# Kernel tuning notes

Hardware: AMD Instinct MI355X
Metric: run time of the kernel (lower is better)

## Reference

```python
import jax, jax.numpy as jnp
import numpy as np

NEG_SLOPE = 0.2  # PyG GATConv default LeakyReLU slope


def _gat(h, src, dst, num_nodes, W, a_src, a_dst, bias):
    """PyG-style GATConv (concat=True, eval mode, self-loops already in src/dst)."""
    heads, out = a_src.shape
    hp = (h @ W).reshape(num_nodes, heads, out)          # (N, H, F)
    e_s = (hp * a_src).sum(-1)                            # (N, H)
    e_d = (hp * a_dst).sum(-1)                            # (N, H)
    e = jax.nn.leaky_relu(e_s[src] + e_d[dst], NEG_SLOPE)  # (E, H)
    m = jax.ops.segment_max(e, dst, num_segments=num_nodes)
    w = jnp.exp(e - m[dst])
    z = jax.ops.segment_sum(w, dst, num_segments=num_nodes)
    alpha = w / (z[dst] + 1e-16)                          # softmax over in-edges per dst
    agg = jax.ops.segment_sum(hp[src] * alpha[:, :, None], dst, num_segments=num_nodes)
    return agg.reshape(num_nodes, heads * out) + bias


def setup_inputs() -> dict:
    key = jax.random.key(0)
    ks = jax.random.split(key, 20)
    N, T, Fin, H, heads, E = 30000, 4, 256, 64, 4, 240000
    D = H * heads  # 256
    s = 0.05
    p = lambda k, shape: (jax.random.normal(k, shape, jnp.float32) * s)
    return {
        "x": jax.random.normal(ks[0], (N, T, Fin), jnp.float32),
        "edge_index": jax.random.randint(ks[1], (2, E), 0, N, jnp.int32),
        "Wp": p(ks[2], (Fin, H)), "bp": p(ks[3], (H,)),
        "W0": p(ks[4], (H, D)), "a_src0": p(ks[5], (heads, H)), "a_dst0": p(ks[6], (heads, H)), "b0": p(ks[7], (D,)),
        "W1": p(ks[8], (D, D)), "a_src1": p(ks[9], (heads, H)), "a_dst1": p(ks[10], (heads, H)), "b1": p(ks[11], (D,)),
        "Wq": p(ks[12], (D, D)), "bq": p(ks[13], (D,)),
        "Wk": p(ks[14], (D, D)), "bk": p(ks[15], (D,)),
        "Wv": p(ks[16], (D, D)), "bv": p(ks[17], (D,)),
    }


def reference(x, edge_index, Wp, bp, W0, a_src0, a_dst0, b0, W1, a_src1, a_dst1, b1,
              Wq, bq, Wk, bk, Wv, bv):
    N, T, Fin = x.shape
    D = Wq.shape[0]
    loops = jnp.arange(N, dtype=edge_index.dtype)
    src = jnp.concatenate([edge_index[0], loops])  # add self-loops (PyG default)
    dst = jnp.concatenate([edge_index[1], loops])
    xT = jnp.transpose(x, (1, 0, 2))  # (T, N, Fin)

    def step(_, xt):
        h = xt @ Wp + bp
        h = jax.nn.elu(_gat(h, src, dst, N, W0, a_src0, a_dst0, b0))
        h = jax.nn.elu(_gat(h, src, dst, N, W1, a_src1, a_dst1, b1))
        return None, h

    _, embs = jax.lax.scan(step, None, xT)  # (T, N, D)

    # temporal attention
    Q = embs @ Wq + bq
    K = embs @ Wk + bk
    V = embs @ Wv + bv
    Q_time = Q.mean(axis=1)  # (T, D)
    K_time = K.mean(axis=1)  # (T, D)
    scores = (Q_time @ K_time.T) / jnp.sqrt(jnp.asarray(D, jnp.float32))
    attn = jax.nn.softmax(scores, axis=1)            # (T, T)
    Vr = V.reshape(T, -1)                            # (T, N*D)
    attended = attn @ Vr                             # (T, N*D)
    return attended[-1].reshape(N, D)
```

## Files before the change

### kernel.cpp

```cpp
#include <hip/hip_runtime.h>
#include <math.h>

#define NEG_SLOPE 0.2f

typedef __attribute__((ext_vector_type(8))) short short8;
typedef __attribute__((ext_vector_type(4))) float f32x4;

__device__ inline unsigned short f2bf(float f){
  union { float f; unsigned u; } v; v.f = f;
  unsigned r = v.u + 0x7fffu + ((v.u >> 16) & 1u);
  return (unsigned short)(r >> 16);
}
__device__ inline float bf2f(unsigned u){
  union { unsigned u; float f; } v; v.u = u << 16; return v.f;
}

__global__ __launch_bounds__(256) void k_deg_count(const int* __restrict__ dst, int E, int* __restrict__ deg){
  int i = blockIdx.x*256 + threadIdx.x;
  if (i < E) atomicAdd(&deg[dst[i]], 1);
}
__global__ __launch_bounds__(256) void k_scan_blk(const int* __restrict__ deg, int* __restrict__ rowptr,
                                                  int* __restrict__ bsum, int N){
  __shared__ int ws[4];
  int tid = threadIdx.x;
  int i = blockIdx.x*256 + tid;
  int v = (i < N) ? deg[i]+1 : 0;
  int lane = tid & 63, w = tid >> 6;
  int s = v;
  #pragma unroll
  for (int off=1; off<64; off<<=1){
    int u = __shfl_up(s, off);
    if (lane >= off) s += u;
  }
  if (lane == 63) ws[w] = s;
  __syncthreads();
  int woff = 0;
  #pragma unroll
  for (int k=0;k<4;k++) if (k < w) woff += ws[k];
  int incl = s + woff;
  if (i < N) rowptr[i] = incl - v;
  if (tid == 255) bsum[blockIdx.x] = incl;
}
__global__ __launch_bounds__(256) void k_scan_top(int* __restrict__ bsum, int nb, int* __restrict__ rowptrN){
  __shared__ int buf[256];
  int tid = threadIdx.x;
  int v = (tid < nb) ? bsum[tid] : 0;
  buf[tid] = v;
  __syncthreads();
  for (int off=1; off<256; off<<=1){
    int add = (tid >= off) ? buf[tid-off] : 0;
    __syncthreads();
    buf[tid] += add;
    __syncthreads();
  }
  if (tid < nb) bsum[tid] = buf[tid] - v;
  if (tid == 0) rowptrN[0] = buf[255];
}
__global__ __launch_bounds__(256) void k_scan_fix(int* __restrict__ rowptr, const int* __restrict__ bsum,
                                                  int* __restrict__ pos, int* __restrict__ colidx, int N){
  int i = blockIdx.x*256 + threadIdx.x;
  if (i < N){
    int r = rowptr[i] + bsum[blockIdx.x];
    rowptr[i] = r;
    colidx[r] = i;
    pos[i] = r + 1;
  }
}
__global__ __launch_bounds__(256) void k_fill_edges(const int* __restrict__ src, const int* __restrict__ dst,
                                                    int E, int* __restrict__ pos, int* __restrict__ colidx){
  int i = blockIdx.x*256 + threadIdx.x;
  if (i < E){
    int d = dst[i];
    colidx[atomicAdd(&pos[d],1)] = src[i];
  }
}

__global__ __launch_bounds__(256) void k_prep(const float* __restrict__ Wp, const float* __restrict__ W0,
                                              const float* __restrict__ W1, const float* __restrict__ Wv,
                                              const float* __restrict__ as0, const float* __restrict__ ad0,
                                              unsigned short* __restrict__ WpT, unsigned short* __restrict__ W0T4,
                                              unsigned short* __restrict__ W1T, unsigned short* __restrict__ WvT,
                                              float* __restrict__ ahs, float* __restrict__ ahd){
  int idx = blockIdx.x*256 + threadIdx.x;
  if (idx < 16384){
    int k = idx >> 6, p = idx & 63;
    WpT[p*256 + k] = f2bf(Wp[idx]);
  } else if (idx < 32768){
    int i = idx - 16384;
    int h = i >> 12, r = i & 4095, p = r >> 6, k = r & 63;
    W0T4[i] = f2bf(W0[k*256 + h*64 + p]);
  } else if (idx < 98304){
    int i = idx - 32768; int k = i >> 8, p = i & 255;
    W1T[p*256 + k] = f2bf(W1[i]);
  } else if (idx < 163840){
    int i = idx - 98304; int k = i >> 8, p = i & 255;
    WvT[p*256 + k] = f2bf(Wv[i]);
  } else if (idx < 164096){
    int i = idx - 163840;
    int h = i >> 6, d = i & 63;
    float ss = 0.f, sd = 0.f;
    for (int j=0;j<64;j++){
      float w = W0[d*256 + h*64 + j];
      ss += w * as0[h*64 + j];
      sd += w * ad0[h*64 + j];
    }
    ahs[i] = ss; ahd[i] = sd;
  }
}

__global__ __launch_bounds__(256) void k_h0(const float* __restrict__ A,
                                            const unsigned short* __restrict__ Bt,
                                            const float* __restrict__ bias,
                                            unsigned short* __restrict__ C, int M, int Nn){
  int wid = blockIdx.x*4 + (threadIdx.x >> 6);
  int m0 = wid * 64;
  if (m0 >= M) return;
  int lane = threadIdx.x & 63;
  int lr = lane & 15, g = lane >> 4, lk = g*8;
  const float* Arow[4];
  #pragma unroll
  for (int m=0;m<4;m++){
    int row = m0 + m*16 + lr;
    if (row > M-1) row = M-1;
    Arow[m] = A + (size_t)row*256 + lk;
  }
  const unsigned short* Bb = Bt + (size_t)lr*256 + lk;
  f32x4 acc[4][4];
  #pragma unroll
  for (int m=0;m<4;m++)
    #pragma unroll
    for (int n=0;n<4;n++)
      #pragma unroll
      for (int j=0;j<4;j++) acc[m][n][j] = 0.f;

  #pragma unroll 2
  for (int ks=0; ks<8; ks++){
    int k0 = ks*32;
    short8 bfr[4];
    #pragma unroll
    for (int n=0;n<4;n++)
      bfr[n] = *(const short8*)(Bb + (size_t)n*16*256 + k0);
    short8 afr[4];
    #pragma unroll
    for (int m=0;m<4;m++){
      float4 u = *(const float4*)(Arow[m] + k0);
      float4 w = *(const float4*)(Arow[m] + k0 + 4);
      afr[m][0]=(short)f2bf(u.x); afr[m][1]=(short)f2bf(u.y);
      afr[m][2]=(short)f2bf(u.z); afr[m][3]=(short)f2bf(u.w);
      afr[m][4]=(short)f2bf(w.x); afr[m][5]=(short)f2bf(w.y);
      afr[m][6]=(short)f2bf(w.z); afr[m][7]=(short)f2bf(w.w);
    }
    #pragma unroll
    for (int m=0;m<4;m++)
      #pragma unroll
      for (int n=0;n<4;n++)
        acc[m][n] = __builtin_amdgcn_mfma_f32_16x16x32_bf16(afr[m], bfr[n], acc[m][n], 0,0,0);
  }
  #pragma unroll
  for (int n=0;n<4;n++){
    int col = n*16 + lr;
    float bcol = bias[col];
    #pragma unroll
    for (int m=0;m<4;m++){
      #pragma unroll
      for (int j=0;j<4;j++){
        int row = m0 + m*16 + g*4 + j;
        if (row < M){
          int t = row & 3, nn = row >> 2;
          C[(size_t)t*Nn*64 + (size_t)nn*64 + col] = f2bf(acc[m][n][j] + bcol);
        }
      }
    }
  }
}

__global__ __launch_bounds__(256) void k_gat0(const unsigned short* __restrict__ A,
                                              const unsigned short* __restrict__ W0T4,
                                              const float* __restrict__ b0,
                                              unsigned short* __restrict__ C, int M){
  int h = blockIdx.y;
  int wid = blockIdx.x*4 + (threadIdx.x >> 6);
  int m0 = wid * 64;
  if (m0 >= M) return;
  int lane = threadIdx.x & 63;
  int lr = lane & 15, g = lane >> 4, lk = g*8;
  const unsigned short* Wh = W0T4 + (size_t)h*64*64;
  f32x4 acc[4][4];
  #pragma unroll
  for (int m=0;m<4;m++)
    #pragma unroll
    for (int n=0;n<4;n++)
      #pragma unroll
      for (int j=0;j<4;j++) acc[m][n][j] = 0.f;

  #pragma unroll
  for (int ks=0; ks<2; ks++){
    short8 bfr[4], afr[4];
    #pragma unroll
    for (int n=0;n<4;n++)
      bfr[n] = *(const short8*)(Wh + (size_t)(n*16+lr)*64 + ks*32 + lk);
    #pragma unroll
    for (int m=0;m<4;m++){
      int row = m0 + m*16 + lr;
      if (row > M-1) row = M-1;
      afr[m] = *(const short8*)(A + (size_t)row*256 + h*64 + ks*32 + lk);
    }
    #pragma unroll
    for (int m=0;m<4;m++)
      #pragma unroll
      for (int n=0;n<4;n++)
        acc[m][n] = __builtin_amdgcn_mfma_f32_16x16x32_bf16(afr[m], bfr[n], acc[m][n], 0,0,0);
  }
  #pragma unroll
  for (int n=0;n<4;n++){
    int col = h*64 + n*16 + lr;
    float bcol = b0[col];
    #pragma unroll
    for (int m=0;m<4;m++){
      #pragma unroll
      for (int j=0;j<4;j++){
        int row = m0 + m*16 + g*4 + j;
        if (row < M){
          float v = acc[m][n][j] + bcol;
          v = (v > 0.f) ? v : (__expf(v) - 1.f);
          C[(size_t)row*256 + col] = f2bf(v);
        }
      }
    }
  }
}

template<int K, bool BIAS, bool CF32>
__global__ __launch_bounds__(512) void k_gemm_p256(const unsigned short* __restrict__ A,
                                                   const unsigned short* __restrict__ Bt,
                                                   const float* __restrict__ bias,
                                                   void* __restrict__ Cv, int M){
  constexpr int BK = 64, PAD = 8;
  __shared__ unsigned short Als[128][BK+PAD];
  __shared__ unsigned short Bls[256][BK+PAD];
  int tid = threadIdx.x;
  int m0  = blockIdx.x * 128;
  int wave = tid >> 6, lane = tid & 63;
  int wr = wave & 3, wc = wave >> 2;
  int lr = lane & 15, lk = (lane >> 4) * 8;
  f32x4 acc[2][8];
  #pragma unroll
  for (int m=0;m<2;m++)
    #pragma unroll
    for (int n=0;n<8;n++)
      #pragma unroll
      for (int j=0;j<4;j++) acc[m][n][j] = 0.f;

  for (int k0 = 0; k0 < K; k0 += BK){
    #pragma unroll
    for (int i=0;i<2;i++){
      int idx = tid + i*512;
      int r = idx >> 3, ch = (idx & 7)*8;
      int row = m0 + r;
      uint4 v = make_uint4(0,0,0,0);
      if (row < M) v = *(const uint4*)(A + (size_t)row*K + k0 + ch);
      *(uint4*)(&Als[r][ch]) = v;
    }
    #pragma unroll
    for (int i=0;i<4;i++){
      int idx = tid + i*512;
      int r = idx >> 3, ch = (idx & 7)*8;
      *(uint4*)(&Bls[r][ch]) = *(const uint4*)(Bt + (size_t)r*K + k0 + ch);
    }
    __syncthreads();
    #pragma unroll
    for (int ks=0; ks<2; ks++){
      short8 afr[2], bfr[8];
      #pragma unroll
      for (int m=0;m<2;m++)
        afr[m] = *(const short8*)(&Als[wr*32 + m*16 + lr][ks*32 + lk]);
      #pragma unroll
      for (int n=0;n<8;n++)
        bfr[n] = *(const short8*)(&Bls[wc*128 + n*16 + lr][ks*32 + lk]);
      #pragma unroll
      for (int m=0;m<2;m++)
        #pragma unroll
        for (int n=0;n<8;n++)
          acc[m][n] = __builtin_amdgcn_mfma_f32_16x16x32_bf16(afr[m], bfr[n], acc[m][n], 0,0,0);
    }
    __syncthreads();
  }
  #pragma unroll
  for (int m=0;m<2;m++){
    #pragma unroll
    for (int n=0;n<8;n++){
      int col = wc*128 + n*16 + lr;
      float bcol = BIAS ? bias[col] : 0.f;
      #pragma unroll
      for (int j=0;j<4;j++){
        int row = m0 + wr*32 + m*16 + (lane>>4)*4 + j;
        if (row < M){
          float v = acc[m][n][j] + bcol;
          if (CF32) ((float*)Cv)[(size_t)row*256 + col] = v;
          else      ((unsigned short*)Cv)[(size_t)row*256 + col] = f2bf(v);
        }
      }
    }
  }
}

__global__ __launch_bounds__(512) void k_gemm_fin(const unsigned short* __restrict__ embs,
                                                  const float* __restrict__ awp,
                                                  const unsigned short* __restrict__ Bt,
                                                  const float* __restrict__ bias,
                                                  float* __restrict__ C, int M){
  constexpr int K = 256, BK = 64, PAD = 8;
  __shared__ unsigned short Als[128][BK+PAD];
  __shared__ unsigned short Bls[256][BK+PAD];
  int tid = threadIdx.x;
  int m0  = blockIdx.x * 128;
  int wave = tid >> 6, lane = tid & 63;
  int wr = wave & 3, wc = wave >> 2;
  int lr = lane & 15, lk = (lane >> 4) * 8;
  float a0=awp[0], a1=awp[1], a2=awp[2], a3=awp[3];
  size_t sl = (size_t)M*256;
  f32x4 acc[2][8];
  #pragma unroll
  for (int m=0;m<2;m++)
    #pragma unroll
    for (int n=0;n<8;n++)
      #pragma unroll
      for (int j=0;j<4;j++) acc[m][n][j] = 0.f;

  for (int k0 = 0; k0 < K; k0 += BK){
    #pragma unroll
    for (int i=0;i<2;i++){
      int idx = tid + i*512;
      int r = idx >> 3, ch = (idx & 7)*8;
      int row = m0 + r;
      uint4 w = make_uint4(0,0,0,0);
      if (row < M){
        size_t o = (size_t)row*256 + k0 + ch;
        uint4 u0 = *(const uint4*)(embs + o);
        uint4 u1 = *(const uint4*)(embs + o + sl);
        uint4 u2 = *(const uint4*)(embs + o + 2*sl);
        uint4 u3 = *(const uint4*)(embs + o + 3*sl);
        const unsigned* p0=&u0.x; const unsigned* p1=&u1.x;
        const unsigned* p2=&u2.x; const unsigned* p3=&u3.x;
        unsigned* pw=&w.x;
        #pragma unroll
        for (int q=0;q<4;q++){
          float lo = a0*bf2f(p0[q]&0xffffu) + a1*bf2f(p1[q]&0xffffu) + a2*bf2f(p2[q]&0xffffu) + a3*bf2f(p3[q]&0xffffu);
          float hi = a0*bf2f(p0[q]>>16)     + a1*bf2f(p1[q]>>16)     + a2*bf2f(p2[q]>>16)     + a3*bf2f(p3[q]>>16);
          pw[q] = (unsigned)f2bf(lo) | ((unsigned)f2bf(hi) << 16);
        }
      }
      *(uint4*)(&Als[r][ch]) = w;
    }
    #pragma unroll
    for (int i=0;i<4;i++){
      int idx = tid + i*512;
      int r = idx >> 3, ch = (idx & 7)*8;
      *(uint4*)(&Bls[r][ch]) = *(const uint4*)(Bt + (size_t)r*K + k0 + ch);
    }
    __syncthreads();
    #pragma unroll
    for (int ks=0; ks<2; ks++){
      short8 afr[2], bfr[8];
      #pragma unroll
      for (int m=0;m<2;m++)
        afr[m] = *(const short8*)(&Als[wr*32 + m*16 + lr][ks*32 + lk]);
      #pragma unroll
      for (int n=0;n<8;n++)
        bfr[n] = *(const short8*)(&Bls[wc*128 + n*16 + lr][ks*32 + lk]);
      #pragma unroll
      for (int m=0;m<2;m++)
        #pragma unroll
        for (int n=0;n<8;n++)
          acc[m][n] = __builtin_amdgcn_mfma_f32_16x16x32_bf16(afr[m], bfr[n], acc[m][n], 0,0,0);
    }
    __syncthreads();
  }
  #pragma unroll
  for (int m=0;m<2;m++){
    #pragma unroll
    for (int n=0;n<8;n++){
      int col = wc*128 + n*16 + lr;
      float bcol = bias[col];
      #pragma unroll
      for (int j=0;j<4;j++){
        int row = m0 + wr*32 + m*16 + (lane>>4)*4 + j;
        if (row < M)
          C[(size_t)row*256 + col] = acc[m][n][j] + bcol;
      }
    }
  }
}

__global__ __launch_bounds__(256) void k_esd0(const unsigned short* __restrict__ h0,
                                              const float* __restrict__ ahs, const float* __restrict__ ahd,
                                              float* __restrict__ e_s, float* __restrict__ e_d, int M){
  int n = blockIdx.x*4 + (threadIdx.x >> 6);
  if (n >= M) return;
  int lane = threadIdx.x & 63;
  int h = lane >> 4, l4 = (lane & 15)*4;
  uint2 v = *(const uint2*)(h0 + (size_t)n*64 + l4);
  float v0 = bf2f(v.x & 0xffffu), v1 = bf2f(v.x >> 16);
  float v2 = bf2f(v.y & 0xffffu), v3 = bf2f(v.y >> 16);
  float4 as = *(const float4*)(ahs + h*64 + l4);
  float4 ad = *(const float4*)(ahd + h*64 + l4);
  float ps = v0*as.x + v1*as.y + v2*as.z + v3*as.w;
  float pd = v0*ad.x + v1*ad.y + v2*ad.z + v3*ad.w;
  #pragma unroll
  for (int off=1; off<16; off<<=1){ ps += __shfl_xor(ps,off); pd += __shfl_xor(pd,off); }
  if ((lane & 15) == 0){
    e_s[n*4+h] = ps; e_d[n*4+h] = pd;
  }
}

__global__ __launch_bounds__(256) void k_agg0(const unsigned short* __restrict__ h0all,
                                              const float* __restrict__ e_s, const float* __restrict__ e_d,
                                              const int* __restrict__ rowptr, const int* __restrict__ colidx,
                                              unsigned short* __restrict__ agg, int N){
  int n = blockIdx.x*4 + (threadIdx.x >> 6);
  if (n >= N) return;
  int t = blockIdx.y;
  int g = t*N + n;
  int lane = threadIdx.x & 63;
  int h = lane >> 4, l4 = (lane & 15)*4;
  int s0 = rowptr[n], s1 = rowptr[n+1];
  float ed = e_d[(size_t)g*4 + h];
  float z = 0.f;
  float a0=0.f, a1=0.f, a2=0.f, a3=0.f;
  const unsigned short* h0t = h0all + (size_t)t*N*64;
  const float* est = e_s + (size_t)t*N*4;
  int i = s0;
  for (; i+4 <= s1; i += 4){
    int sA = colidx[i], sB = colidx[i+1], sC = colidx[i+2], sD = colidx[i+3];
    uint2 vA = *(const uint2*)(h0t + (size_t)sA*64 + l4);
    uint2 vB = *(const uint2*)(h0t + (size_t)sB*64 + l4);
    uint2 vC = *(const uint2*)(h0t + (size_t)sC*64 + l4);
    uint2 vD = *(const uint2*)(h0t + (size_t)sD*64 + l4);
    float eA = est[sA*4+h] + ed, eB = est[sB*4+h] + ed, eC = est[sC*4+h] + ed, eD = est[sD*4+h] + ed;
    eA = (eA>0.f)?eA:NEG_SLOPE*eA; eB = (eB>0.f)?eB:NEG_SLOPE*eB;
    eC = (eC>0.f)?eC:NEG_SLOPE*eC; eD = (eD>0.f)?eD:NEG_SLOPE*eD;
    float wA = __expf(eA), wB = __expf(eB), wC = __expf(eC), wD = __expf(eD);
    z += (wA + wB) + (wC + wD);
    a0 += wA*bf2f(vA.x&0xffffu) + wB*bf2f(vB.x&0xffffu) + wC*bf2f(vC.x&0xffffu) + wD*bf2f(vD.x&0xffffu);
    a1 += wA*bf2f(vA.x>>16)     + wB*bf2f(vB.x>>16)     + wC*bf2f(vC.x>>16)     + wD*bf2f(vD.x>>16);
    a2 += wA*bf2f(vA.y&0xffffu) + wB*bf2f(vB.y&0xffffu) + wC*bf2f(vC.y&0xffffu) + wD*bf2f(vD.y&0xffffu);
    a3 += wA*bf2f(vA.y>>16)     + wB*bf2f(vB.y>>16)     + wC*bf2f(vC.y>>16)     + wD*bf2f(vD.y>>16);
  }
  for (; i < s1; ++i){
    int s = colidx[i];
    float e = est[s*4 + h] + ed;
    e = (e > 0.f) ? e : NEG_SLOPE*e;
    float w = __expf(e);
    z += w;
    uint2 v = *(const uint2*)(h0t + (size_t)s*64 + l4);
    a0 += w * bf2f(v.x & 0xffffu);
    a1 += w * bf2f(v.x >> 16);
    a2 += w * bf2f(v.y & 0xffffu);
    a3 += w * bf2f(v.y >> 16);
  }
  float inv = 1.f / (z + 1e-16f);
  unsigned lo = (unsigned)f2bf(a0*inv) | ((unsigned)f2bf(a1*inv) << 16);
  unsigned hi = (unsigned)f2bf(a2*inv) | ((unsigned)f2bf(a3*inv) << 16);
  *(uint2*)(agg + (size_t)g*256 + h*64 + l4) = make_uint2(lo, hi);
}

__global__ __launch_bounds__(256) void k_esd(const unsigned short* __restrict__ hp,
                                             const float* __restrict__ a_s, const float* __restrict__ a_d,
                                             float* __restrict__ e_s, float* __restrict__ e_d, int M){
  int n = blockIdx.x*4 + (threadIdx.x >> 6);
  if (n >= M) return;
  int lane = threadIdx.x & 63;
  uint2 v = *(const uint2*)(hp + (size_t)n*256 + lane*4);
  float v0 = bf2f(v.x & 0xffffu), v1 = bf2f(v.x >> 16);
  float v2 = bf2f(v.y & 0xffffu), v3 = bf2f(v.y >> 16);
  float4 as = *(const float4*)(a_s + lane*4);
  float4 ad = *(const float4*)(a_d + lane*4);
  float ps = v0*as.x + v1*as.y + v2*as.z + v3*as.w;
  float pd = v0*ad.x + v1*ad.y + v2*ad.z + v3*ad.w;
  #pragma unroll
  for (int off=1; off<16; off<<=1){ ps += __shfl_xor(ps,off); pd += __shfl_xor(pd,off); }
  if ((lane & 15) == 0){
    int h = lane >> 4;
    e_s[n*4+h] = ps; e_d[n*4+h] = pd;
  }
}

__global__ __launch_bounds__(256) void k_agg(const unsigned short* __restrict__ hpall,
                                             const float* __restrict__ e_s, const float* __restrict__ e_d,
                                             const int* __restrict__ rowptr, const int* __restrict__ colidx,
                                             const float* __restrict__ bias, unsigned short* __restrict__ outb,
                                             int N){
  int n = blockIdx.x*4 + (threadIdx.x >> 6);
  if (n >= N) return;
  int t = blockIdx.y;
  int g = t*N + n;
  int lane = threadIdx.x & 63;
  int h = lane >> 4;
  int s0 = rowptr[n], s1 = rowptr[n+1];
  float ed = e_d[(size_t)g*4 + h];
  float z = 0.f;
  float a0=0.f, a1=0.f, a2=0.f, a3=0.f;
  const unsigned short* hpt = hpall + (size_t)t*N*256;
  const float* est = e_s + (size_t)t*N*4;
  int i = s0;
  for (; i+4 <= s1; i += 4){
    int sA = colidx[i], sB = colidx[i+1], sC = colidx[i+2], sD = colidx[i+3];
    uint2 vA = *(const uint2*)(hpt + (size_t)sA*256 + lane*4);
    uint2 vB = *(const uint2*)(hpt + (size_t)sB*256 + lane*4);
    uint2 vC = *(const uint2*)(hpt + (size_t)sC*256 + lane*4);
    uint2 vD = *(const uint2*)(hpt + (size_t)sD*256 + lane*4);
    float eA = est[sA*4+h] + ed, eB = est[sB*4+h] + ed, eC = est[sC*4+h] + ed, eD = est[sD*4+h] + ed;
    eA = (eA>0.f)?eA:NEG_SLOPE*eA; eB = (eB>0.f)?eB:NEG_SLOPE*eB;
    eC = (eC>0.f)?eC:NEG_SLOPE*eC; eD = (eD>0.f)?eD:NEG_SLOPE*eD;
    float wA = __expf(eA), wB = __expf(eB), wC = __expf(eC), wD = __expf(eD);
    z += (wA + wB) + (wC + wD);
    a0 += wA*bf2f(vA.x&0xffffu) + wB*bf2f(vB.x&0xffffu) + wC*bf2f(vC.x&0xffffu) + wD*bf2f(vD.x&0xffffu);
    a1 += wA*bf2f(vA.x>>16)     + wB*bf2f(vB.x>>16)     + wC*bf2f(vC.x>>16)     + wD*bf2f(vD.x>>16);
    a2 += wA*bf2f(vA.y&0xffffu) + wB*bf2f(vB.y&0xffffu) + wC*bf2f(vC.y&0xffffu) + wD*bf2f(vD.y&0xffffu);
    a3 += wA*bf2f(vA.y>>16)     + wB*bf2f(vB.y>>16)     + wC*bf2f(vC.y>>16)     + wD*bf2f(vD.y>>16);
  }
  for (; i < s1; ++i){
    int s = colidx[i];
    float e = est[s*4 + h] + ed;
    e = (e > 0.f) ? e : NEG_SLOPE*e;
    float w = __expf(e);
    z += w;
    uint2 v = *(const uint2*)(hpt + (size_t)s*256 + lane*4);
    a0 += w * bf2f(v.x & 0xffffu);
    a1 += w * bf2f(v.x >> 16);
    a2 += w * bf2f(v.y & 0xffffu);
    a3 += w * bf2f(v.y >> 16);
  }
  float inv = 1.f / (z + 1e-16f);
  float4 b = *(const float4*)(bias + lane*4);
  float o0 = a0*inv + b.x, o1 = a1*inv + b.y, o2 = a2*inv + b.z, o3 = a3*inv + b.w;
  o0 = (o0 > 0.f) ? o0 : (__expf(o0) - 1.f);
  o1 = (o1 > 0.f) ? o1 : (__expf(o1) - 1.f);
  o2 = (o2 > 0.f) ? o2 : (__expf(o2) - 1.f);
  o3 = (o3 > 0.f) ? o3 : (__expf(o3) - 1.f);
  unsigned lo = (unsigned)f2bf(o0) | ((unsigned)f2bf(o1) << 16);
  unsigned hi = (unsigned)f2bf(o2) | ((unsigned)f2bf(o3) << 16);
  *(uint2*)(outb + (size_t)g*256 + lane*4) = make_uint2(lo, hi);
}

__global__ __launch_bounds__(256) void k_colsum(const unsigned short* __restrict__ emb, float* __restrict__ sums, int N){
  __shared__ float red[8][256];
  int tid = threadIdx.x;
  int t = blockIdx.x >> 6, chunk = blockIdx.x & 63;
  int rows_per = (N + 63) / 64;
  int r0 = chunk * rows_per;
  int r1 = min(N, r0 + rows_per);
  const unsigned short* base = emb + (size_t)t*N*256;
  int c0 = (tid & 31)*8, rg = tid >> 5;
  float s[8] = {0,0,0,0,0,0,0,0};
  for (int r = r0 + rg; r < r1; r += 8){
    uint4 v = *(const uint4*)(base + (size_t)r*256 + c0);
    s[0] += bf2f(v.x & 0xffffu); s[1] += bf2f(v.x >> 16);
    s[2] += bf2f(v.y & 0xffffu); s[3] += bf2f(v.y >> 16);
    s[4] += bf2f(v.z & 0xffffu); s[5] += bf2f(v.z >> 16);
    s[6] += bf2f(v.w & 0xffffu); s[7] += bf2f(v.w >> 16);
  }
  #pragma unroll
  for (int j=0;j<8;j++) red[rg][c0+j] = s[j];
  __syncthreads();
  float tot = 0.f;
  #pragma unroll
  for (int g=0;g<8;g++) tot += red[g][tid];
  atomicAdd(&sums[t*256 + tid], tot);
}

__global__ __launch_bounds__(256) void k_attn(const float* __restrict__ sum_emb,
                                              const float* __restrict__ Wq, const float* __restrict__ bq,
                                              const float* __restrict__ Wk, const float* __restrict__ bk,
                                              float* __restrict__ aw, int N){
  __shared__ float mean_s[4][256];
  __shared__ float red[256];
  __shared__ float scores_s[4];
  int j = threadIdx.x;
  float invN = 1.0f/(float)N;
  #pragma unroll
  for (int t=0;t<4;t++) mean_s[t][j] = sum_emb[t*256+j]*invN;
  __syncthreads();
  float q3 = bq[j];
  float kt0=bk[j], kt1=bk[j], kt2=bk[j], kt3=bk[j];
  for (int m=0;m<256;m++){
    float wq = Wq[m*256+j];
    float wk = Wk[m*256+j];
    float m0 = mean_s[0][m], m1 = mean_s[1][m], m2 = mean_s[2][m], m3 = mean_s[3][m];
    q3  += m3*wq;
    kt0 += m0*wk; kt1 += m1*wk; kt2 += m2*wk; kt3 += m3*wk;
  }
  float kts0=kt0, kts1=kt1, kts2=kt2, kts3=kt3;
  #pragma unroll
  for (int t=0;t<4;t++){
    float ktv = (t==0)?kts0:((t==1)?kts1:((t==2)?kts2:kts3));
    red[j] = q3*ktv;
    __syncthreads();
    for (int off=128; off>0; off>>=1){
      if (j < off) red[j] += red[j+off];
      __syncthreads();
    }
    if (j==0) scores_s[t] = red[0]*(1.0f/16.0f);
    __syncthreads();
  }
  if (j==0){
    float mx = fmaxf(fmaxf(scores_s[0],scores_s[1]),fmaxf(scores_s[2],scores_s[3]));
    float w0 = __expf(scores_s[0]-mx), w1 = __expf(scores_s[1]-mx),
          w2 = __expf(scores_s[2]-mx), w3 = __expf(scores_s[3]-mx);
    float s = w0+w1+w2+w3;
    aw[0]=w0/s; aw[1]=w1/s; aw[2]=w2/s; aw[3]=w3/s;
  }
}

extern "C" void kernel_launch(void* const* d_in, const int* in_sizes, int n_in,
                              void* d_out, int out_size, void* d_ws, size_t ws_size,
                              hipStream_t stream){
  (void)n_in; (void)out_size; (void)ws_size;
  const float* x   = (const float*)d_in[0];
  const int*   ei  = (const int*)d_in[1];
  const float* Wp  = (const float*)d_in[2];
  const float* bp  = (const float*)d_in[3];
  const float* W0  = (const float*)d_in[4];
  const float* as0 = (const float*)d_in[5];
  const float* ad0 = (const float*)d_in[6];
  const float* b0  = (const float*)d_in[7];
  const float* W1  = (const float*)d_in[8];
  const float* as1 = (const float*)d_in[9];
  const float* ad1 = (const float*)d_in[10];
  const float* b1  = (const float*)d_in[11];
  const float* Wq  = (const float*)d_in[12];
  const float* bq  = (const float*)d_in[13];
  const float* Wk  = (const float*)d_in[14];
  const float* bk  = (const float*)d_in[15];
  const float* Wv  = (const float*)d_in[16];
  const float* bv  = (const float*)d_in[17];
  float* out = (float*)d_out;

  const int T = 4, FIN = 256;
  const int N = in_sizes[0] / (T*FIN);
  const int E = in_sizes[1] / 2;
  const int TN = T*N;
  const int* src = ei;
  const int* dst = ei + E;

  char* ws = (char*)d_ws;
  size_t cur = 0;
  auto alloc = [&](size_t bytes)->void*{
    void* p = ws + cur;
    cur += (bytes + 255) & ~(size_t)255;
    return p;
  };
  unsigned short* h0all = (unsigned short*)alloc((size_t)TN*64*2);
  unsigned short* bufA  = (unsigned short*)alloc((size_t)TN*256*2);
  unsigned short* bufB  = (unsigned short*)alloc((size_t)TN*256*2);
  unsigned short* embs  = (unsigned short*)alloc((size_t)TN*256*2);
  float* e_s    = (float*)alloc((size_t)TN*4*4);
  float* e_d    = (float*)alloc((size_t)TN*4*4);
  float* sume   = (float*)alloc(4*256*4);
  float* aw     = (float*)alloc(256);
  float* ah0s   = (float*)alloc(256*4);
  float* ah0d   = (float*)alloc(256*4);
  int*   rowptr = (int*)alloc((size_t)(N+1)*4);
  int*   deg    = (int*)alloc((size_t)N*4);
  int*   pos    = (int*)alloc((size_t)N*4);
  int*   bsum   = (int*)alloc((size_t)256*4);
  int*   colidx = (int*)alloc((size_t)(E+N)*4);
  unsigned short* WpT  = (unsigned short*)alloc((size_t)64*256*2);
  unsigned short* W0T4 = (unsigned short*)alloc((size_t)4*64*64*2);
  unsigned short* W1T  = (unsigned short*)alloc((size_t)256*256*2);
  unsigned short* WvT  = (unsigned short*)alloc((size_t)256*256*2);

  int nb256 = (N+255)/256;
  int nbE   = (E+255)/256;
  int gm4   = (TN+127)/128;
  int gmN   = (N+127)/128;
  int gagg  = (TN+3)/4;

  hipMemsetAsync(deg, 0, (size_t)N*4, stream);
  k_deg_count<<<nbE,256,0,stream>>>(dst, E, deg);
  k_scan_blk<<<nb256,256,0,stream>>>(deg, rowptr, bsum, N);
  k_scan_top<<<1,256,0,stream>>>(bsum, nb256, rowptr + N);
  k_scan_fix<<<nb256,256,0,stream>>>(rowptr, bsum, pos, colidx, N);
  k_fill_edges<<<nbE,256,0,stream>>>(src, dst, E, pos, colidx);
  hipMemsetAsync(sume, 0, 4*256*4, stream);

  k_prep<<<641,256,0,stream>>>(Wp, W0, W1, Wv, as0, ad0, WpT, W0T4, W1T, WvT, ah0s, ah0d);

  k_h0<<<(TN/64+3)/4 + 1,256,0,stream>>>(x, WpT, bp, h0all, TN, N);

  k_esd0<<<gagg,256,0,stream>>>(h0all, ah0s, ah0d, e_s, e_d, TN);
  k_agg0<<<dim3((N+3)/4, T),256,0,stream>>>(h0all, e_s, e_d, rowptr, colidx, bufA, N);
  k_gat0<<<dim3((TN+255)/256, 4),256,0,stream>>>(bufA, W0T4, b0, bufB, TN);
  k_gemm_p256<256,false,false><<<gm4,512,0,stream>>>(bufB, W1T, nullptr, bufA, TN);
  k_esd<<<gagg,256,0,stream>>>(bufA, as1, ad1, e_s, e_d, TN);
  k_agg<<<dim3((N+3)/4, T),256,0,stream>>>(bufA, e_s, e_d, rowptr, colidx, b1, embs, N);
  k_colsum<<<256,256,0,stream>>>(embs, sume, N);

  k_attn<<<1,256,0,stream>>>(sume, Wq, bq, Wk, bk, aw, N);
  k_gemm_fin<<<gmN,512,0,stream>>>(embs, aw, WvT, bv, out, N);
}
```

Measured before the change: 457.4 us.

## Fuse GAT0 projection with layer-1 GEMM and vectorize edge aggregation loops

Merges the per-head layer-0 transform (with bias and ELU) and the layer-1 256x256 projection into one kernel. The intermediate activation tile stays in shared memory, so the bf16 round trip through global memory and one launch go away. The two aggregation kernels now split each wave into two halves that each take alternate edges with 16-byte loads, then combine the halves with a cross-half shuffle. In exchange, the fused kernel uses a smaller 64-row tile and reloads W1 per block, and half the lanes sit idle in the aggregation epilogue.

```diff
diff --git a/kernel.cpp b/kernel.cpp
--- a/kernel.cpp
+++ b/kernel.cpp
@@ -174,132 +174,85 @@
   }
 }
 
-__global__ __launch_bounds__(256) void k_gat0(const unsigned short* __restrict__ A,
-                                              const unsigned short* __restrict__ W0T4,
-                                              const float* __restrict__ b0,
-                                              unsigned short* __restrict__ C, int M){
-  int h = blockIdx.y;
-  int wid = blockIdx.x*4 + (threadIdx.x >> 6);
-  int m0 = wid * 64;
-  if (m0 >= M) return;
-  int lane = threadIdx.x & 63;
-  int lr = lane & 15, g = lane >> 4, lk = g*8;
-  const unsigned short* Wh = W0T4 + (size_t)h*64*64;
-  f32x4 acc[4][4];
-  #pragma unroll
-  for (int m=0;m<4;m++)
-    #pragma unroll
-    for (int n=0;n<4;n++)
-      #pragma unroll
-      for (int j=0;j<4;j++) acc[m][n][j] = 0.f;
-
-  #pragma unroll
-  for (int ks=0; ks<2; ks++){
-    short8 bfr[4], afr[4];
-    #pragma unroll
-    for (int n=0;n<4;n++)
-      bfr[n] = *(const short8*)(Wh + (size_t)(n*16+lr)*64 + ks*32 + lk);
-    #pragma unroll
-    for (int m=0;m<4;m++){
-      int row = m0 + m*16 + lr;
-      if (row > M-1) row = M-1;
-      afr[m] = *(const short8*)(A + (size_t)row*256 + h*64 + ks*32 + lk);
-    }
-    #pragma unroll
-    for (int m=0;m<4;m++)
-      #pragma unroll
-      for (int n=0;n<4;n++)
-        acc[m][n] = __builtin_amdgcn_mfma_f32_16x16x32_bf16(afr[m], bfr[n], acc[m][n], 0,0,0);
-  }
-  #pragma unroll
-  for (int n=0;n<4;n++){
-    int col = h*64 + n*16 + lr;
+__global__ __launch_bounds__(256) void k_gat01(const unsigned short* __restrict__ A,
+                                               const unsigned short* __restrict__ W0T4,
+                                               const float* __restrict__ b0,
+                                               const unsigned short* __restrict__ W1T,
+                                               unsigned short* __restrict__ hp, int M){
+  __shared__ unsigned short H1[64][264];
+  __shared__ unsigned short Bls[256][72];
+  int tid = threadIdx.x;
+  int m0 = blockIdx.x * 64;
+  int wave = tid >> 6, lane = tid & 63;
+  int lr = lane & 15, g4 = lane >> 4, lk = g4*8;
+  int rbase = m0 + wave*16;
+
+  f32x4 acc1[16];
+  #pragma unroll
+  for (int q=0;q<16;q++)
+    #pragma unroll
+    for (int j=0;j<4;j++) acc1[q][j] = 0.f;
+  int arow = rbase + lr; if (arow > M-1) arow = M-1;
+  #pragma unroll
+  for (int h=0;h<4;h++){
+    short8 afr[2];
+    #pragma unroll
+    for (int ks=0;ks<2;ks++)
+      afr[ks] = *(const short8*)(A + (size_t)arow*256 + h*64 + ks*32 + lk);
+    #pragma unroll
+    for (int nn=0;nn<4;nn++){
+      #pragma unroll
+      for (int ks=0;ks<2;ks++){
+        short8 bfr = *(const short8*)(W0T4 + ((size_t)h*64 + nn*16 + lr)*64 + ks*32 + lk);
+        acc1[h*4+nn] = __builtin_amdgcn_mfma_f32_16x16x32_bf16(afr[ks], bfr, acc1[h*4+nn], 0,0,0);
+      }
+    }
+  }
+  #pragma unroll
+  for (int q=0;q<16;q++){
+    int col = q*16 + lr;
     float bcol = b0[col];
     #pragma unroll
-    for (int m=0;m<4;m++){
-      #pragma unroll
-      for (int j=0;j<4;j++){
-        int row = m0 + m*16 + g*4 + j;
-        if (row < M){
-          float v = acc[m][n][j] + bcol;
-          v = (v > 0.f) ? v : (__expf(v) - 1.f);
-          C[(size_t)row*256 + col] = f2bf(v);
-        }
+    for (int j=0;j<4;j++){
+      float v = acc1[q][j] + bcol;
+      v = (v > 0.f) ? v : (__expf(v) - 1.f);
+      H1[wave*16 + g4*4 + j][col] = f2bf(v);
+    }
+  }
+  __syncthreads();
+
+  f32x4 acc2[16];
+  #pragma unroll
+  for (int q=0;q<16;q++)
+    #pragma unroll
+    for (int j=0;j<4;j++) acc2[q][j] = 0.f;
+  for (int k0=0;k0<256;k0+=64){
+    #pragma unroll
+    for (int it=0; it<8; it++){
+      int idx = tid + it*256;
+      int p = idx >> 3, ch = (idx & 7)*8;
+      *(uint4*)(&Bls[p][ch]) = *(const uint4*)(W1T + (size_t)p*256 + k0 + ch);
+    }
+    __syncthreads();
+    #pragma unroll
+    for (int ks=0;ks<2;ks++){
+      short8 afr = *(const short8*)(&H1[wave*16 + lr][k0 + ks*32 + lk]);
+      #pragma unroll
+      for (int q=0;q<16;q++){
+        short8 bfr = *(const short8*)(&Bls[q*16 + lr][ks*32 + lk]);
+        acc2[q] = __builtin_amdgcn_mfma_f32_16x16x32_bf16(afr, bfr, acc2[q], 0,0,0);
       }
     }
-  }
-}
-
-template<int K, bool BIAS, bool CF32>
-__global__ __launch_bounds__(512) void k_gemm_p256(const unsigned short* __restrict__ A,
-                                                   const unsigned short* __restrict__ Bt,
-                                                   const float* __restrict__ bias,
-                                                   void* __restrict__ Cv, int M){
-  constexpr int BK = 64, PAD = 8;
-  __shared__ unsigned short Als[128][BK+PAD];
-  __shared__ unsigned short Bls[256][BK+PAD];
-  int tid = threadIdx.x;
-  int m0  = blockIdx.x * 128;
-  int wave = tid >> 6, lane = tid & 63;
-  int wr = wave & 3, wc = wave >> 2;
-  int lr = lane & 15, lk = (lane >> 4) * 8;
-  f32x4 acc[2][8];
-  #pragma unroll
-  for (int m=0;m<2;m++)
-    #pragma unroll
-    for (int n=0;n<8;n++)
-      #pragma unroll
-      for (int j=0;j<4;j++) acc[m][n][j] = 0.f;
-
-  for (int k0 = 0; k0 < K; k0 += BK){
-    #pragma unroll
-    for (int i=0;i<2;i++){
-      int idx = tid + i*512;
-      int r = idx >> 3, ch = (idx & 7)*8;
-      int row = m0 + r;
-      uint4 v = make_uint4(0,0,0,0);
-      if (row < M) v = *(const uint4*)(A + (size_t)row*K + k0 + ch);
-      *(uint4*)(&Als[r][ch]) = v;
-    }
-    #pragma unroll
-    for (int i=0;i<4;i++){
-      int idx = tid + i*512;
-      int r = idx >> 3, ch = (idx & 7)*8;
-      *(uint4*)(&Bls[r][ch]) = *(const uint4*)(Bt + (size_t)r*K + k0 + ch);
-    }
-    __syncthreads();
-    #pragma unroll
-    for (int ks=0; ks<2; ks++){
-      short8 afr[2], bfr[8];
-      #pragma unroll
-      for (int m=0;m<2;m++)
-        afr[m] = *(const short8*)(&Als[wr*32 + m*16 + lr][ks*32 + lk]);
-      #pragma unroll
-      for (int n=0;n<8;n++)
-        bfr[n] = *(const short8*)(&Bls[wc*128 + n*16 + lr][ks*32 + lk]);
-      #pragma unroll
-      for (int m=0;m<2;m++)
-        #pragma unroll
-        for (int n=0;n<8;n++)
-          acc[m][n] = __builtin_amdgcn_mfma_f32_16x16x32_bf16(afr[m], bfr[n], acc[m][n], 0,0,0);
-    }
-    __syncthreads();
-  }
-  #pragma unroll
-  for (int m=0;m<2;m++){
-    #pragma unroll
-    for (int n=0;n<8;n++){
-      int col = wc*128 + n*16 + lr;
-      float bcol = BIAS ? bias[col] : 0.f;
-      #pragma unroll
-      for (int j=0;j<4;j++){
-        int row = m0 + wr*32 + m*16 + (lane>>4)*4 + j;
-        if (row < M){
-          float v = acc[m][n][j] + bcol;
-          if (CF32) ((float*)Cv)[(size_t)row*256 + col] = v;
-          else      ((unsigned short*)Cv)[(size_t)row*256 + col] = f2bf(v);
-        }
-      }
+    __syncthreads();
+  }
+  #pragma unroll
+  for (int q=0;q<16;q++){
+    int col = q*16 + lr;
+    #pragma unroll
+    for (int j=0;j<4;j++){
+      int row = m0 + wave*16 + g4*4 + j;
+      if (row < M)
+        hp[(size_t)row*256 + col] = f2bf(acc2[q][j]);
     }
   }
 }
@@ -422,46 +375,51 @@
   int t = blockIdx.y;
   int g = t*N + n;
   int lane = threadIdx.x & 63;
-  int h = lane >> 4, l4 = (lane & 15)*4;
+  int half = lane >> 5, l = lane & 31;
+  int h = l >> 3, di = (l & 7)*8;
   int s0 = rowptr[n], s1 = rowptr[n+1];
   float ed = e_d[(size_t)g*4 + h];
-  float z = 0.f;
-  float a0=0.f, a1=0.f, a2=0.f, a3=0.f;
   const unsigned short* h0t = h0all + (size_t)t*N*64;
   const float* est = e_s + (size_t)t*N*4;
+  float z = 0.f;
+  float a[8] = {0,0,0,0,0,0,0,0};
   int i = s0;
-  for (; i+4 <= s1; i += 4){
-    int sA = colidx[i], sB = colidx[i+1], sC = colidx[i+2], sD = colidx[i+3];
-    uint2 vA = *(const uint2*)(h0t + (size_t)sA*64 + l4);
-    uint2 vB = *(const uint2*)(h0t + (size_t)sB*64 + l4);
-    uint2 vC = *(const uint2*)(h0t + (size_t)sC*64 + l4);
-    uint2 vD = *(const uint2*)(h0t + (size_t)sD*64 + l4);
-    float eA = est[sA*4+h] + ed, eB = est[sB*4+h] + ed, eC = est[sC*4+h] + ed, eD = est[sD*4+h] + ed;
-    eA = (eA>0.f)?eA:NEG_SLOPE*eA; eB = (eB>0.f)?eB:NEG_SLOPE*eB;
-    eC = (eC>0.f)?eC:NEG_SLOPE*eC; eD = (eD>0.f)?eD:NEG_SLOPE*eD;
-    float wA = __expf(eA), wB = __expf(eB), wC = __expf(eC), wD = __expf(eD);
-    z += (wA + wB) + (wC + wD);
-    a0 += wA*bf2f(vA.x&0xffffu) + wB*bf2f(vB.x&0xffffu) + wC*bf2f(vC.x&0xffffu) + wD*bf2f(vD.x&0xffffu);
-    a1 += wA*bf2f(vA.x>>16)     + wB*bf2f(vB.x>>16)     + wC*bf2f(vC.x>>16)     + wD*bf2f(vD.x>>16);
-    a2 += wA*bf2f(vA.y&0xffffu) + wB*bf2f(vB.y&0xffffu) + wC*bf2f(vC.y&0xffffu) + wD*bf2f(vD.y&0xffffu);
-    a3 += wA*bf2f(vA.y>>16)     + wB*bf2f(vB.y>>16)     + wC*bf2f(vC.y>>16)     + wD*bf2f(vD.y>>16);
-  }
-  for (; i < s1; ++i){
-    int s = colidx[i];
+  for (; i+2 <= s1; i += 2){
+    int s = colidx[i + half];
+    uint4 v = *(const uint4*)(h0t + (size_t)s*64 + di);
     float e = est[s*4 + h] + ed;
-    e = (e > 0.f) ? e : NEG_SLOPE*e;
+    e = fmaxf(e, NEG_SLOPE*e);
     float w = __expf(e);
     z += w;
-    uint2 v = *(const uint2*)(h0t + (size_t)s*64 + l4);
-    a0 += w * bf2f(v.x & 0xffffu);
-    a1 += w * bf2f(v.x >> 16);
-    a2 += w * bf2f(v.y & 0xffffu);
-    a3 += w * bf2f(v.y >> 16);
-  }
-  float inv = 1.f / (z + 1e-16f);
-  unsigned lo = (unsigned)f2bf(a0*inv) | ((unsigned)f2bf(a1*inv) << 16);
-  unsigned hi = (unsigned)f2bf(a2*inv) | ((unsigned)f2bf(a3*inv) << 16);
-  *(uint2*)(agg + (size_t)g*256 + h*64 + l4) = make_uint2(lo, hi);
+    a[0] += w*bf2f(v.x&0xffffu); a[1] += w*bf2f(v.x>>16);
+    a[2] += w*bf2f(v.y&0xffffu); a[3] += w*bf2f(v.y>>16);
+    a[4] += w*bf2f(v.z&0xffffu); a[5] += w*bf2f(v.z>>16);
+    a[6] += w*bf2f(v.w&0xffffu); a[7] += w*bf2f(v.w>>16);
+  }
+  if (i < s1 && half == 0){
+    int s = colidx[i];
+    uint4 v = *(const uint4*)(h0t + (size_t)s*64 + di);
+    float e = est[s*4 + h] + ed;
+    e = fmaxf(e, NEG_SLOPE*e);
+    float w = __expf(e);
+    z += w;
+    a[0] += w*bf2f(v.x&0xffffu); a[1] += w*bf2f(v.x>>16);
+    a[2] += w*bf2f(v.y&0xffffu); a[3] += w*bf2f(v.y>>16);
+    a[4] += w*bf2f(v.z&0xffffu); a[5] += w*bf2f(v.z>>16);
+    a[6] += w*bf2f(v.w&0xffffu); a[7] += w*bf2f(v.w>>16);
+  }
+  z += __shfl_xor(z, 32);
+  #pragma unroll
+  for (int q=0;q<8;q++) a[q] += __shfl_xor(a[q], 32);
+  if (half == 0){
+    float inv = 1.f / (z + 1e-16f);
+    uint4 r;
+    r.x = (unsigned)f2bf(a[0]*inv) | ((unsigned)f2bf(a[1]*inv) << 16);
+    r.y = (unsigned)f2bf(a[2]*inv) | ((unsigned)f2bf(a[3]*inv) << 16);
+    r.z = (unsigned)f2bf(a[4]*inv) | ((unsigned)f2bf(a[5]*inv) << 16);
+    r.w = (unsigned)f2bf(a[6]*inv) | ((unsigned)f2bf(a[7]*inv) << 16);
+    *(uint4*)(agg + (size_t)g*256 + l*8) = r;
+  }
 }
 
 __global__ __launch_bounds__(256) void k_esd(const unsigned short* __restrict__ hp,
@@ -495,52 +453,58 @@
   int t = blockIdx.y;
   int g = t*N + n;
   int lane = threadIdx.x & 63;
-  int h = lane >> 4;
+  int half = lane >> 5, l = lane & 31;
+  int h = l >> 3, d0 = l*8;
   int s0 = rowptr[n], s1 = rowptr[n+1];
   float ed = e_d[(size_t)g*4 + h];
-  float z = 0.f;
-  float a0=0.f, a1=0.f, a2=0.f, a3=0.f;
   const unsigned short* hpt = hpall + (size_t)t*N*256;
   const float* est = e_s + (size_t)t*N*4;
+  float z = 0.f;
+  float a[8] = {0,0,0,0,0,0,0,0};
   int i = s0;
-  for (; i+4 <= s1; i += 4){
-    int sA = colidx[i], sB = colidx[i+1], sC = colidx[i+2], sD = colidx[i+3];
-    uint2 vA = *(const uint2*)(hpt + (size_t)sA*256 + lane*4);
-    uint2 vB = *(const uint2*)(hpt + (size_t)sB*256 + lane*4);
-    uint2 vC = *(const uint2*)(hpt + (size_t)sC*256 + lane*4);
-    uint2 vD = *(const uint2*)(hpt + (size_t)sD*256 + lane*4);
-    float eA = est[sA*4+h] + ed, eB = est[sB*4+h] + ed, eC = est[sC*4+h] + ed, eD = est[sD*4+h] + ed;
-    eA = (eA>0.f)?eA:NEG_SLOPE*eA; eB = (eB>0.f)?eB:NEG_SLOPE*eB;
-    eC = (eC>0.f)?eC:NEG_SLOPE*eC; eD = (eD>0.f)?eD:NEG_SLOPE*eD;
-    float wA = __expf(eA), wB = __expf(eB), wC = __expf(eC), wD = __expf(eD);
-    z += (wA + wB) + (wC + wD);
-    a0 += wA*bf2f(vA.x&0xffffu) + wB*bf2f(vB.x&0xffffu) + wC*bf2f(vC.x&0xffffu) + wD*bf2f(vD.x&0xffffu);
-    a1 += wA*bf2f(vA.x>>16)     + wB*bf2f(vB.x>>16)     + wC*bf2f(vC.x>>16)     + wD*bf2f(vD.x>>16);
-    a2 += wA*bf2f(vA.y&0xffffu) + wB*bf2f(vB.y&0xffffu) + wC*bf2f(vC.y&0xffffu) + wD*bf2f(vD.y&0xffffu);
-    a3 += wA*bf2f(vA.y>>16)     + wB*bf2f(vB.y>>16)     + wC*bf2f(vC.y>>16)     + wD*bf2f(vD.y>>16);
-  }
-  for (; i < s1; ++i){
-    int s = colidx[i];
+  for (; i+2 <= s1; i += 2){
+    int s = colidx[i + half];
+    uint4 v = *(const uint4*)(hpt + (size_t)s*256 + d0);
     float e = est[s*4 + h] + ed;
-    e = (e > 0.f) ? e : NEG_SLOPE*e;
+    e = fmaxf(e, NEG_SLOPE*e);
     float w = __expf(e);
     z += w;
-    uint2 v = *(const uint2*)(hpt + (size_t)s*256 + lane*4);
-    a0 += w * bf2f(v.x & 0xffffu);
-    a1 += w * bf2f(v.x >> 16);
-    a2 += w * bf2f(v.y & 0xffffu);
-    a3 += w * bf2f(v.y >> 16);
-  }
-  float inv = 1.f / (z + 1e-16f);
-  float4 b = *(const float4*)(bias + lane*4);
-  float o0 = a0*inv + b.x, o1 = a1*inv + b.y, o2 = a2*inv + b.z, o3 = a3*inv + b.w;
-  o0 = (o0 > 0.f) ? o0 : (__expf(o0) - 1.f);
-  o1 = (o1 > 0.f) ? o1 : (__expf(o1) - 1.f);
-  o2 = (o2 > 0.f) ? o2 : (__expf(o2) - 1.f);
-  o3 = (o3 > 0.f) ? o3 : (__expf(o3) - 1.f);
-  unsigned lo = (unsigned)f2bf(o0) | ((unsigned)f2bf(o1) << 16);
-  unsigned hi = (unsigned)f2bf(o2) | ((unsigned)f2bf(o3) << 16);
-  *(uint2*)(outb + (size_t)g*256 + lane*4) = make_uint2(lo, hi);
+    a[0] += w*bf2f(v.x&0xffffu); a[1] += w*bf2f(v.x>>16);
+    a[2] += w*bf2f(v.y&0xffffu); a[3] += w*bf2f(v.y>>16);
+    a[4] += w*bf2f(v.z&0xffffu); a[5] += w*bf2f(v.z>>16);
+    a[6] += w*bf2f(v.w&0xffffu); a[7] += w*bf2f(v.w>>16);
+  }
+  if (i < s1 && half == 0){
+    int s = colidx[i];
+    uint4 v = *(const uint4*)(hpt + (size_t)s*256 + d0);
+    float e = est[s*4 + h] + ed;
+    e = fmaxf(e, NEG_SLOPE*e);
+    float w = __expf(e);
+    z += w;
+    a[0] += w*bf2f(v.x&0xffffu); a[1] += w*bf2f(v.x>>16);
+    a[2] += w*bf2f(v.y&0xffffu); a[3] += w*bf2f(v.y>>16);
+    a[4] += w*bf2f(v.z&0xffffu); a[5] += w*bf2f(v.z>>16);
+    a[6] += w*bf2f(v.w&0xffffu); a[7] += w*bf2f(v.w>>16);
+  }
+  z += __shfl_xor(z, 32);
+  #pragma unroll
+  for (int q=0;q<8;q++) a[q] += __shfl_xor(a[q], 32);
+  if (half == 0){
+    float inv = 1.f / (z + 1e-16f);
+    float4 bA = *(const float4*)(bias + d0);
+    float4 bB = *(const float4*)(bias + d0 + 4);
+    float o[8];
+    o[0]=a[0]*inv+bA.x; o[1]=a[1]*inv+bA.y; o[2]=a[2]*inv+bA.z; o[3]=a[3]*inv+bA.w;
+    o[4]=a[4]*inv+bB.x; o[5]=a[5]*inv+bB.y; o[6]=a[6]*inv+bB.z; o[7]=a[7]*inv+bB.w;
+    #pragma unroll
+    for (int q=0;q<8;q++) o[q] = (o[q] > 0.f) ? o[q] : (__expf(o[q]) - 1.f);
+    uint4 r;
+    r.x = (unsigned)f2bf(o[0]) | ((unsigned)f2bf(o[1]) << 16);
+    r.y = (unsigned)f2bf(o[2]) | ((unsigned)f2bf(o[3]) << 16);
+    r.z = (unsigned)f2bf(o[4]) | ((unsigned)f2bf(o[5]) << 16);
+    r.w = (unsigned)f2bf(o[6]) | ((unsigned)f2bf(o[7]) << 16);
+    *(uint4*)(outb + (size_t)g*256 + d0) = r;
+  }
 }
 
 __global__ __launch_bounds__(256) void k_colsum(const unsigned short* __restrict__ emb, float* __restrict__ sums, int N){
@@ -672,7 +636,6 @@
 
   int nb256 = (N+255)/256;
   int nbE   = (E+255)/256;
-  int gm4   = (TN+127)/128;
   int gmN   = (N+127)/128;
   int gagg  = (TN+3)/4;
 
@@ -690,10 +653,9 @@
 
   k_esd0<<<gagg,256,0,stream>>>(h0all, ah0s, ah0d, e_s, e_d, TN);
   k_agg0<<<dim3((N+3)/4, T),256,0,stream>>>(h0all, e_s, e_d, rowptr, colidx, bufA, N);
-  k_gat0<<<dim3((TN+255)/256, 4),256,0,stream>>>(bufA, W0T4, b0, bufB, TN);
-  k_gemm_p256<256,false,false><<<gm4,512,0,stream>>>(bufB, W1T, nullptr, bufA, TN);
-  k_esd<<<gagg,256,0,stream>>>(bufA, as1, ad1, e_s, e_d, TN);
-  k_agg<<<dim3((N+3)/4, T),256,0,stream>>>(bufA, e_s, e_d, rowptr, colidx, b1, embs, N);
+  k_gat01<<<(TN+63)/64,256,0,stream>>>(bufA, W0T4, b0, W1T, bufB, TN);
+  k_esd<<<gagg,256,0,stream>>>(bufB, as1, ad1, e_s, e_d, TN);
+  k_agg<<<dim3((N+3)/4, T),256,0,stream>>>(bufB, e_s, e_d, rowptr, colidx, b1, embs, N);
   k_colsum<<<256,256,0,stream>>>(embs, sume, N);
 
   k_attn<<<1,256,0,stream>>>(sume, Wq, bq, Wk, bk, aw, N);
```

Measured after the change: 445.0 us. 1.03x faster.
